# Kernel tuning notes

Hardware: AMD Instinct MI355X
Metric: run time of the kernel (lower is better)

The kernel has to match this reference:

```python
import jax, jax.numpy as jnp
import numpy as np

BS, N_LINKS, MAX_LEN = 8192, 512, 32
D_LINK, D_PATH, D_READ, N_OUT = 32, 128, 256, 3
BN_EPS = 1e-5


def setup_inputs() -> dict:
    key = jax.random.key(0)
    ks = jax.random.split(key, 16)
    capa = jax.random.uniform(ks[0], (BS, N_LINKS), jnp.float32, 0.5, 1.0) * 100.0
    avail = jax.random.uniform(ks[1], (BS, N_LINKS), jnp.float32) * capa
    loss = jax.random.uniform(ks[2], (BS, N_LINKS), jnp.float32) * 0.05
    demand = jax.random.uniform(ks[3], (BS,), jnp.float32) * 10.0
    path = jax.random.randint(ks[4], (BS, MAX_LEN), 0, N_LINKS)
    hop_num = jax.random.randint(ks[5], (BS,), 1, MAX_LEN + 1)
    s = 0.1
    inp = {
        "demand": demand,
        "link_avail_capacity": avail,
        "link_capacity": capa,
        "link_loss": loss,
        "path": path,
        "hop_num": hop_num,
        # GRU params (PyTorch layout: [3H, D] gates ordered r,z,n)
        "gru_w_ih": jax.random.normal(ks[6], (3 * D_PATH, D_LINK), jnp.float32) * s,
        "gru_w_hh": jax.random.normal(ks[7], (3 * D_PATH, D_PATH), jnp.float32) * s,
        "gru_b_ih": jax.random.normal(ks[8], (3 * D_PATH,), jnp.float32) * s,
        "gru_b_hh": jax.random.normal(ks[9], (3 * D_PATH,), jnp.float32) * s,
        "bn_gamma": jnp.ones((D_PATH,), jnp.float32),
        "bn_beta": jnp.zeros((D_PATH,), jnp.float32),
        # stacked readout heads [N_OUT, ...]
        "rW1": jax.random.normal(ks[10], (N_OUT, D_PATH, D_READ), jnp.float32) * s,
        "rb1": jnp.zeros((N_OUT, D_READ), jnp.float32),
        "rW2": jax.random.normal(ks[11], (N_OUT, D_READ, D_READ), jnp.float32) * s,
        "rb2": jnp.zeros((N_OUT, D_READ), jnp.float32),
        "rW3": jax.random.normal(ks[12], (N_OUT, D_READ, 1), jnp.float32) * s,
        "rb3": jnp.zeros((N_OUT, 1), jnp.float32),
    }
    return inp


def _gru_scan(x_bt, h0, w_ih, w_hh, b_ih, b_hh):
    # x_bt: [B, T, D]; h0: [B, H] -> outputs [B, T, H]
    H = h0.shape[-1]
    def step(h, x_t):
        gi = x_t @ w_ih.T + b_ih          # [B, 3H]
        gh = h @ w_hh.T + b_hh            # [B, 3H]
        i_r, i_z, i_n = gi[:, :H], gi[:, H:2*H], gi[:, 2*H:]
        h_r, h_z, h_n = gh[:, :H], gh[:, H:2*H], gh[:, 2*H:]
        r = jax.nn.sigmoid(i_r + h_r)
        z = jax.nn.sigmoid(i_z + h_z)
        n = jnp.tanh(i_n + r * h_n)
        h_new = (1.0 - z) * n + z * h
        return h_new, h_new
    _, outs = jax.lax.scan(step, h0, jnp.swapaxes(x_bt, 0, 1))
    return jnp.swapaxes(outs, 0, 1)


def reference(demand, link_avail_capacity, link_capacity, link_loss, path, hop_num,
              gru_w_ih, gru_w_hh, gru_b_ih, gru_b_hh, bn_gamma, bn_beta,
              rW1, rb1, rW2, rb2, rW3, rb3):
    bs, n_links = link_capacity.shape
    max_len = path.shape[1]
    max_capa = jax.lax.stop_gradient(jnp.max(link_capacity))
    # link_state: [B, n_links, D_LINK]; first D_LINK-4 channels are zeros
    feats = jnp.stack([
        link_avail_capacity / max_capa,
        link_capacity / max_capa,
        link_avail_capacity / link_capacity,
        link_loss,
    ], axis=-1)
    link_state = jnp.concatenate(
        [jnp.zeros((bs, n_links, D_LINK - 4), feats.dtype), feats], axis=-1)
    link_state = jax.lax.stop_gradient(link_state)  # original detaches
    # initial hidden: zeros except last channel = demand/max_capa
    h0 = jnp.concatenate(
        [jnp.zeros((bs, D_PATH - 1), feats.dtype), (demand / max_capa)[:, None]], axis=-1)
    # fused gather of link states along each path, masked past hop_num
    gathered = jnp.take_along_axis(link_state, path[:, :, None], axis=1)  # [B, T, D]
    mask = (jnp.arange(max_len)[None, :] < hop_num[:, None])[:, :, None]
    link_inputs = gathered * mask.astype(gathered.dtype)
    outputs = _gru_scan(link_inputs, h0, gru_w_ih, gru_w_hh, gru_b_ih, gru_b_hh)
    # extract hidden state at last hop of each path
    idx = (hop_num - 1)[:, None, None]
    flow = jnp.take_along_axis(outputs, idx, axis=1)[:, 0, :]  # [B, H]
    # BatchNorm1d (training mode: batch statistics, biased variance)
    mean = jnp.mean(flow, axis=0)
    var = jnp.mean((flow - mean) ** 2, axis=0)
    flow = (flow - mean) * jax.lax.rsqrt(var + BN_EPS) * bn_gamma + bn_beta
    # readout heads: Linear -> SELU -> Linear -> SELU -> Linear
    h1 = jax.nn.selu(jnp.einsum('bh,uhr->ubr', flow, rW1) + rb1[:, None, :])
    h2 = jax.nn.selu(jnp.einsum('ubr,urs->ubs', h1, rW2) + rb2[:, None, :])
    y = jnp.einsum('ubs,uso->ubo', h2, rW3) + rb3[:, None, :]  # [U, B, 1]
    return jnp.transpose(y[:, :, 0], (1, 0))  # [B, U]
```

## Files before the change

### kernel.cpp

```cpp
#include <hip/hip_runtime.h>


#define BS 8192
#define NL 512
#define ML 32
#define DP 128
#define DR 256
#define NJOB 512
#define ST 172

#define OFF_SUM    64
#define OFF_SSQ    192
#define OFF_CUR    576
#define OFF_PERM   640
#define OFF_WHH16  (OFF_PERM + BS)
#define OFF_W1     (OFF_WHH16 + 24576)
#define OFF_W2     (OFF_W1 + 49152)
#define OFF_FEATS  (OFF_W2 + 98304)
#define OFF_FLOW   (OFF_FEATS + BS*ML*4)

#define FEATS_BLOCKS 1024
#define MAX_BLOCKS   256
#define WPREP_BLOCKS 336
#define SORT_BID     (FEATS_BLOCKS + MAX_BLOCKS + WPREP_BLOCKS)
#define SORT_BLOCKS  32
#define PREP_GRID    (SORT_BID + SORT_BLOCKS)

#define KS (-1.44269504088896340736f)
#define KT ( 2.88539008177792681472f)

typedef _Float16 f16x8 __attribute__((ext_vector_type(8)));
typedef _Float16 f16x4 __attribute__((ext_vector_type(4)));
typedef float    f32x4 __attribute__((ext_vector_type(4)));

__device__ __forceinline__ float exp2_raw_(float x){
#if __has_builtin(__builtin_amdgcn_exp2f)
  return __builtin_amdgcn_exp2f(x);
#else
  return exp2f(x);
#endif
}

__device__ __forceinline__ float sig2_(float x){
  return __builtin_amdgcn_rcpf(1.0f + exp2_raw_(x));
}
__device__ __forceinline__ float tanh2_(float v){
  return fmaf(-2.0f, __builtin_amdgcn_rcpf(1.0f + exp2_raw_(v)), 1.0f);
}
__device__ __forceinline__ float seluf_(float x){
  const float sc = 1.0507009873554805f, al = 1.6732632423543772f;
  return x > 0.0f ? sc*x : sc*al*(__expf(x)-1.0f);
}

__global__ void prep_all(const int* __restrict__ path, const int* __restrict__ hop,
                         const float* __restrict__ avail, const float* __restrict__ capa,
                         const float* __restrict__ loss, const float* __restrict__ whh,
                         const float* __restrict__ rW1, const float* __restrict__ rW2,
                         float* ws){
  const int bid = blockIdx.x;
  const int tid = threadIdx.x;

  if (bid < FEATS_BLOCKS){
    int idx = bid*256 + tid;
    int b = idx >> 5, t = idx & 31;
    f16x4 o = (f16x4)0;
    if (t < hop[b]){
      int l = path[idx];
      float a = avail[b*NL + l];
      float c = capa [b*NL + l];
      o[0] = (_Float16)a;
      o[1] = (_Float16)c;
      o[2] = (_Float16)(a / c);
      o[3] = (_Float16)loss[b*NL + l];
    }
    ((f16x4*)((_Float16*)(ws + OFF_FEATS)))[idx] = o;
  } else if (bid < FEATS_BLOCKS + MAX_BLOCKS){
    const float4* c4 = (const float4*)capa;
    const int n4 = BS*NL/4;
    float m = 0.0f;
    for (int i = (bid - FEATS_BLOCKS)*256 + tid; i < n4; i += MAX_BLOCKS*256){
      float4 v = c4[i];
      m = fmaxf(m, fmaxf(fmaxf(v.x, v.y), fmaxf(v.z, v.w)));
    }
    #pragma unroll
    for (int o = 32; o > 0; o >>= 1) m = fmaxf(m, __shfl_down(m, o, 64));
    if ((tid & 63) == 0) atomicMax((int*)ws, __float_as_int(m));
  } else if (bid < SORT_BID){
    _Float16* whh16 = (_Float16*)(ws + OFF_WHH16);
    _Float16* w1    = (_Float16*)(ws + OFF_W1);
    _Float16* w2    = (_Float16*)(ws + OFF_W2);
    int base = (bid - FEATS_BLOCKS - MAX_BLOCKS)*1024 + tid*4;
    if (base < 49152){
      const float s = (base < 32768) ? KS : KT;
      const float4 v = *(const float4*)(whh + base);
      f16x4 o = { (_Float16)(v.x*s), (_Float16)(v.y*s),
                  (_Float16)(v.z*s), (_Float16)(v.w*s) };
      *(f16x4*)(whh16 + base) = o;
    } else if (base < 147456){
      int j = base - 49152;
      int u = j >> 15;        int rem  = j & 32767;
      int ngrp = rem >> 11;   int rem2 = rem & 2047;
      int kc   = rem2 >> 9;   int rem3 = rem2 & 511;
      int l    = rem3 >> 3;   int e0   = rem3 & 7;
      int n = ngrp*16 + (l & 15);
      int k = kc*32 + (l >> 4)*8 + e0;
      const float* src = rW1 + u*32768 + k*256 + n;
      f16x4 o = { (_Float16)src[0], (_Float16)src[256], (_Float16)src[512], (_Float16)src[768] };
      *(f16x4*)(w1 + j) = o;
    } else {
      int j = base - 147456;
      int u = j >> 16;        int rem  = j & 65535;
      int ngrp = rem >> 12;   int rem2 = rem & 4095;
      int kc   = rem2 >> 9;   int rem3 = rem2 & 511;
      int l    = rem3 >> 3;   int e0   = rem3 & 7;
      int n = ngrp*16 + (l & 15);
      int k = kc*32 + (l >> 4)*8 + e0;
      const float* src = rW2 + u*65536 + k*256 + n;
      f16x4 o = { (_Float16)src[0], (_Float16)src[256], (_Float16)src[512], (_Float16)src[768] };
      *(f16x4*)(w2 + j) = o;
    }
  } else {
    const int v  = bid - SORT_BID;
    const int hv = 32 - v;
    __shared__ int wsum[4];
    __shared__ int cur;
    if (v == 0)
      for (int i = 64 + tid; i < 640; i += 256) ws[i] = 0.0f;
    int cnt = 0;
    for (int b = tid; b < BS; b += 256) cnt += (hop[b] > hv) ? 1 : 0;
    #pragma unroll
    for (int o = 32; o > 0; o >>= 1) cnt += __shfl_down(cnt, o, 64);
    if ((tid & 63) == 0) wsum[tid >> 6] = cnt;
    if (tid == 0) cur = 0;
    __syncthreads();
    const int start_v = wsum[0] + wsum[1] + wsum[2] + wsum[3];
    int* perm = (int*)ws + OFF_PERM;
    for (int b = tid; b < BS; b += 256){
      if (hop[b] == hv){
        int p = atomicAdd(&cur, 1);
        perm[start_v + p] = b;
      }
    }
  }
}

__launch_bounds__(256, 2)
__global__ void kgru(const float* __restrict__ demand, const int* __restrict__ hop,
                     const float* __restrict__ wih, const float* __restrict__ bih,
                     const float* __restrict__ bhh, float* __restrict__ ws,
                     float* __restrict__ flow){
  __shared__ _Float16 hA[2][16*ST];
  const int tid  = threadIdx.x;
  const int w    = tid >> 6;
  const int lane = tid & 63;
  const int lm   = lane & 15;
  const int qd   = lane >> 4;
  const int ch0  = w*32 + lm;
  const int ch1  = w*32 + 16 + lm;
  const float inv_maxc = 1.0f / ws[0];
  const int* perm = (const int*)ws + OFF_PERM;
  const f16x4* feats16 = (const f16x4*)((const _Float16*)(ws + OFF_FEATS));
  const _Float16* whh16 = (const _Float16*)(ws + OFF_WHH16);

  const int bid = blockIdx.x;
  const int q = (bid < 256) ? bid : 767 - bid;

  for (int idx = tid; idx < 1024; idx += 256){
    const int buf = idx >> 9;
    const int rem = idx & 511;
    const int m   = rem >> 5;
    const int c   = 128 + (rem & 31);
    hA[buf][m*ST + c] = (_Float16)0.f;
  }

  f16x8 bfr[2][5], bfz[2][5], bfnh[2][4], bfni[2];
  #pragma unroll
  for (int s = 0; s < 2; ++s){
    const int chs = w*32 + s*16 + lm;
    #pragma unroll
    for (int kc = 0; kc < 4; ++kc){
      bfr[s][kc]  = *(const f16x8*)(whh16 + (      chs)*128 + kc*32 + qd*8);
      bfz[s][kc]  = *(const f16x8*)(whh16 + (128 + chs)*128 + kc*32 + qd*8);
      bfnh[s][kc] = *(const f16x8*)(whh16 + (256 + chs)*128 + kc*32 + qd*8);
    }
    bfr[s][4] = (f16x8)0; bfz[s][4] = (f16x8)0; bfni[s] = (f16x8)0;
    if (qd == 0){
      #pragma unroll
      for (int j = 0; j < 4; ++j){
        float sc = (j < 2) ? inv_maxc : 1.0f;
        bfr[s][4][j] = (_Float16)(wih[(      chs)*32 + 28 + j] * sc * KS);
        bfz[s][4][j] = (_Float16)(wih[(128 + chs)*32 + 28 + j] * sc * KS);
        bfni[s][j]   = (_Float16)(wih[(256 + chs)*32 + 28 + j] * sc * KT);
      }
    }
  }
  const float bR0  = (bih[ch0]     + bhh[ch0]    ) * KS;
  const float bR1  = (bih[ch1]     + bhh[ch1]    ) * KS;
  const float bZ0  = (bih[128+ch0] + bhh[128+ch0]) * KS;
  const float bZ1  = (bih[128+ch1] + bhh[128+ch1]) * KS;
  const float bNI0 = bih[256+ch0] * KT;
  const float bNI1 = bih[256+ch1] * KT;
  const float bNH0 = bhh[256+ch0] * KT;
  const float bNH1 = bhh[256+ch1] * KT;

  int it[4], hp[4];
  #pragma unroll
  for (int r = 0; r < 4; ++r){
    it[r] = perm[q*16 + qd*4 + r];
    hp[r] = hop[it[r]];
  }
  int tmax = max(max(hp[0],hp[1]), max(hp[2],hp[3]));
  tmax = max(tmax, __shfl_xor(tmax, 16, 64));
  tmax = max(tmax, __shfl_xor(tmax, 32, 64));

  const int  fw_i = w*4 + lane;
  const bool fw   = (lane < 4);
  const int  fw_b = fw ? perm[q*16 + fw_i] : 0;

  __syncthreads();

  float hprev0[4], hprev1[4];
  #pragma unroll
  for (int r = 0; r < 4; ++r){
    hprev0[r] = 0.0f;
    hprev1[r] = (ch1 == 127) ? demand[it[r]] * inv_maxc : 0.0f;
    hA[0][(qd*4 + r)*ST + ch0] = (_Float16)hprev0[r];
    hA[0][(qd*4 + r)*ST + ch1] = (_Float16)hprev1[r];
  }
  f16x4 fvreg = (f16x4)0;
  if (fw){
    *(f16x4*)(&hA[0][fw_i*ST + 128]) = feats16[fw_b*ML + 0];
    fvreg = feats16[fw_b*ML + 1];
  }
  __syncthreads();

  for (int t = 0; t < tmax; ++t){
    const int cur = t & 1, nxt = cur ^ 1;
    if (fw){
      *(f16x4*)(&hA[nxt][fw_i*ST + 128]) = fvreg;
      int tn = t + 2; tn = (tn < ML) ? tn : (ML - 1);
      fvreg = feats16[fw_b*ML + tn];
    }

    f16x8 a[5];
    #pragma unroll
    for (int kc = 0; kc < 5; ++kc)
      a[kc] = *(const f16x8*)(&hA[cur][lm*ST + kc*32 + qd*8]);

    {
      f32x4 accr  = {bR0, bR0, bR0, bR0};
      f32x4 accz  = {bZ0, bZ0, bZ0, bZ0};
      f32x4 accnh = {bNH0, bNH0, bNH0, bNH0};
      f32x4 accni = {bNI0, bNI0, bNI0, bNI0};
      #pragma unroll
      for (int kc = 0; kc < 5; ++kc){
        accr = __builtin_amdgcn_mfma_f32_16x16x32_f16(a[kc], bfr[0][kc], accr, 0, 0, 0);
        accz = __builtin_amdgcn_mfma_f32_16x16x32_f16(a[kc], bfz[0][kc], accz, 0, 0, 0);
        if (kc < 4)
          accnh = __builtin_amdgcn_mfma_f32_16x16x32_f16(a[kc], bfnh[0][kc], accnh, 0, 0, 0);
        else
          accni = __builtin_amdgcn_mfma_f32_16x16x32_f16(a[kc], bfni[0], accni, 0, 0, 0);
      }
      #pragma unroll
      for (int r = 0; r < 4; ++r){
        float rr = sig2_(accr[r]);
        float zz = sig2_(accz[r]);
        float nn = tanh2_(fmaf(rr, accnh[r], accni[r]));
        float hn = fmaf(zz, hprev0[r] - nn, nn);
        if (t < hp[r]) hprev0[r] = hn;
        hA[nxt][(qd*4 + r)*ST + ch0] = (_Float16)hprev0[r];
      }
    }
    {
      f32x4 accr  = {bR1, bR1, bR1, bR1};
      f32x4 accz  = {bZ1, bZ1, bZ1, bZ1};
      f32x4 accnh = {bNH1, bNH1, bNH1, bNH1};
      f32x4 accni = {bNI1, bNI1, bNI1, bNI1};
      #pragma unroll
      for (int kc = 0; kc < 5; ++kc){
        accr = __builtin_amdgcn_mfma_f32_16x16x32_f16(a[kc], bfr[1][kc], accr, 0, 0, 0);
        accz = __builtin_amdgcn_mfma_f32_16x16x32_f16(a[kc], bfz[1][kc], accz, 0, 0, 0);
        if (kc < 4)
          accnh = __builtin_amdgcn_mfma_f32_16x16x32_f16(a[kc], bfnh[1][kc], accnh, 0, 0, 0);
        else
          accni = __builtin_amdgcn_mfma_f32_16x16x32_f16(a[kc], bfni[1], accni, 0, 0, 0);
      }
      #pragma unroll
      for (int r = 0; r < 4; ++r){
        float rr = sig2_(accr[r]);
        float zz = sig2_(accz[r]);
        float nn = tanh2_(fmaf(rr, accnh[r], accni[r]));
        float hn = fmaf(zz, hprev1[r] - nn, nn);
        if (t < hp[r]) hprev1[r] = hn;
        hA[nxt][(qd*4 + r)*ST + ch1] = (_Float16)hprev1[r];
      }
    }
    __syncthreads();
  }

  float s0 = 0.f, q0 = 0.f, s1 = 0.f, q1 = 0.f;
  #pragma unroll
  for (int r = 0; r < 4; ++r){
    float v0 = hprev0[r], v1 = hprev1[r];
    flow[it[r]*DP + ch0] = v0;
    flow[it[r]*DP + ch1] = v1;
    s0 += v0;  q0 = fmaf(v0, v0, q0);
    s1 += v1;  q1 = fmaf(v1, v1, q1);
  }
  s0 += __shfl_xor(s0, 16, 64);  s0 += __shfl_xor(s0, 32, 64);
  q0 += __shfl_xor(q0, 16, 64);  q0 += __shfl_xor(q0, 32, 64);
  s1 += __shfl_xor(s1, 16, 64);  s1 += __shfl_xor(s1, 32, 64);
  q1 += __shfl_xor(q1, 16, 64);  q1 += __shfl_xor(q1, 32, 64);
  if (qd == 0){
    atomicAdd(&ws[OFF_SUM + ch0], s0);
    atomicAdd(&ws[OFF_SSQ + ch0], q0);
    atomicAdd(&ws[OFF_SUM + ch1], s1);
    atomicAdd(&ws[OFF_SSQ + ch1], q1);
  }
}

__launch_bounds__(256, 4)
__global__ void kmlp(const float* __restrict__ flow, const float* __restrict__ ws,
                     const float* __restrict__ gamma, const float* __restrict__ beta,
                     const float* __restrict__ rb1, const float* __restrict__ rb2,
                     const float* __restrict__ rW3, const float* __restrict__ rb3,
                     float* __restrict__ out){
  __shared__ _Float16 x_lds[32*136];
  __shared__ _Float16 h1_lds[32*264];
  __shared__ float aa[DP], bb[DP];
  __shared__ float y_part[4][32];
  const int tid  = threadIdx.x;
  const int w    = tid >> 6;
  const int lane = tid & 63;
  const int lm   = lane & 15;
  const int qd   = lane >> 4;
  const int b0   = blockIdx.x * 32;
  const int u    = blockIdx.y;
  const _Float16* w1 = (const _Float16*)(ws + OFF_W1) + u*(DR*DP);
  const _Float16* w2 = (const _Float16*)(ws + OFF_W2) + u*(DR*DR);

  if (tid < DP){
    float m = ws[OFF_SUM + tid] * (1.0f/BS);
    float q = ws[OFF_SSQ + tid] * (1.0f/BS);
    float rstd = rsqrtf(q - m*m + 1e-5f);
    float a = rstd * gamma[tid];
    aa[tid] = a;
    bb[tid] = fmaf(-m, a, beta[tid]);
  }
  __syncthreads();

  for (int idx = tid; idx < 32*DP; idx += 256){
    int i = idx >> 7, h = idx & 127;
    x_lds[i*136 + h] = (_Float16)fmaf(flow[(b0 + i)*DP + h], aa[h], bb[h]);
  }
  __syncthreads();

  for (int nt = 0; nt < 4; ++nt){
    const int ng = 4*w + nt;
    const int n  = ng*16 + lm;
    const float bias1 = rb1[u*DR + n];
    f16x8 b1[4];
    #pragma unroll
    for (int kc = 0; kc < 4; ++kc)
      b1[kc] = *(const f16x8*)(w1 + ((ng*4 + kc)*64 + lane)*8);
    #pragma unroll
    for (int mt = 0; mt < 2; ++mt){
      f32x4 acc = {bias1, bias1, bias1, bias1};
      #pragma unroll
      for (int kc = 0; kc < 4; ++kc){
        f16x8 a1 = *(const f16x8*)(&x_lds[(mt*16 + lm)*136 + kc*32 + qd*8]);
        acc = __builtin_amdgcn_mfma_f32_16x16x32_f16(a1, b1[kc], acc, 0, 0, 0);
      }
      #pragma unroll
      for (int r = 0; r < 4; ++r)
        h1_lds[(mt*16 + qd*4 + r)*264 + n] = (_Float16)seluf_(acc[r]);
    }
  }
  __syncthreads();

  {
    float p[2][4] = {{0.f,0.f,0.f,0.f},{0.f,0.f,0.f,0.f}};
    for (int nt = 0; nt < 4; ++nt){
      const int ng = 4*w + nt;
      const int n  = ng*16 + lm;
      const float bias2 = rb2[u*DR + n];
      const float w3l   = rW3[u*DR + n];
      f16x8 b2[8];
      #pragma unroll
      for (int kc = 0; kc < 8; ++kc)
        b2[kc] = *(const f16x8*)(w2 + ((ng*8 + kc)*64 + lane)*8);
      #pragma unroll
      for (int mt = 0; mt < 2; ++mt){
        f32x4 acc = {bias2, bias2, bias2, bias2};
        #pragma unroll
        for (int kc = 0; kc < 8; ++kc){
          f16x8 a2 = *(const f16x8*)(&h1_lds[(mt*16 + lm)*264 + kc*32 + qd*8]);
          acc = __builtin_amdgcn_mfma_f32_16x16x32_f16(a2, b2[kc], acc, 0, 0, 0);
        }
        #pragma unroll
        for (int r = 0; r < 4; ++r)
          p[mt][r] += seluf_(acc[r]) * w3l;
      }
    }
    #pragma unroll
    for (int mt = 0; mt < 2; ++mt){
      #pragma unroll
      for (int r = 0; r < 4; ++r){
        float v = p[mt][r];
        v += __shfl_xor(v, 1, 64);
        v += __shfl_xor(v, 2, 64);
        v += __shfl_xor(v, 4, 64);
        v += __shfl_xor(v, 8, 64);
        if (lm == 0) y_part[w][mt*16 + qd*4 + r] = v;
      }
    }
  }
  __syncthreads();
  if (tid < 32){
    float y = y_part[0][tid] + y_part[1][tid] + y_part[2][tid] + y_part[3][tid] + rb3[u];
    out[(b0 + tid)*3 + u] = y;
  }
}

extern "C" void kernel_launch(void* const* d_in, const int* in_sizes, int n_in,
                              void* d_out, int out_size, void* d_ws, size_t ws_size,
                              hipStream_t stream){
  const float* demand = (const float*)d_in[0];
  const float* avail  = (const float*)d_in[1];
  const float* capa   = (const float*)d_in[2];
  const float* loss   = (const float*)d_in[3];
  const int*   path   = (const int*)d_in[4];
  const int*   hop    = (const int*)d_in[5];
  const float* wih    = (const float*)d_in[6];
  const float* whh    = (const float*)d_in[7];
  const float* bih    = (const float*)d_in[8];
  const float* bhh    = (const float*)d_in[9];
  const float* gamma  = (const float*)d_in[10];
  const float* beta   = (const float*)d_in[11];
  const float* rW1    = (const float*)d_in[12];
  const float* rb1    = (const float*)d_in[13];
  const float* rW2    = (const float*)d_in[14];
  const float* rb2    = (const float*)d_in[15];
  const float* rW3    = (const float*)d_in[16];
  const float* rb3    = (const float*)d_in[17];
  float* ws  = (float*)d_ws;
  float* out = (float*)d_out;

  prep_all <<<PREP_GRID, 256, 0, stream>>>(path, hop, avail, capa, loss,
                                           whh, rW1, rW2, ws);
  kgru     <<<NJOB, 256, 0, stream>>>(demand, hop, wih, bih, bhh, ws, ws + OFF_FLOW);
  kmlp     <<<dim3(BS/32, 3), 256, 0, stream>>>(ws + OFF_FLOW, ws, gamma, beta,
                                                rb1, rb2, rW3, rb3, out);
}
```

Before: 188.6 us.

## Fuse per-path link feature gather and readout weight repack into GRU kernel

The link-state gather along each path moves out of the prep kernel and into the GRU kernel. Each block gathers the features for its 16 sorted items straight into shared memory, which removes the global fp16 feature buffer write and read-back. The readout W1/W2 fp16 repacking also moves into the GRU blocks, so the prep grid shrinks to the max reduction, Whh conversion and the sort. In exchange, every GRU block pays an uncached random gather before its recurrence starts. Masking of timesteps past hop_num is dropped, which relies on only the hop-1 output being extracted.

```diff
diff --git a/kernel.cpp b/kernel.cpp
--- a/kernel.cpp
+++ b/kernel.cpp
@@ -19,10 +19,9 @@
 #define OFF_FEATS  (OFF_W2 + 98304)
 #define OFF_FLOW   (OFF_FEATS + BS*ML*4)
 
-#define FEATS_BLOCKS 1024
 #define MAX_BLOCKS   256
-#define WPREP_BLOCKS 336
-#define SORT_BID     (FEATS_BLOCKS + MAX_BLOCKS + WPREP_BLOCKS)
+#define WHH_BLOCKS   48
+#define SORT_BID     (MAX_BLOCKS + WHH_BLOCKS)
 #define SORT_BLOCKS  32
 #define PREP_GRID    (SORT_BID + SORT_BLOCKS)
 
@@ -60,25 +59,11 @@
   const int bid = blockIdx.x;
   const int tid = threadIdx.x;
 
-  if (bid < FEATS_BLOCKS){
-    int idx = bid*256 + tid;
-    int b = idx >> 5, t = idx & 31;
-    f16x4 o = (f16x4)0;
-    if (t < hop[b]){
-      int l = path[idx];
-      float a = avail[b*NL + l];
-      float c = capa [b*NL + l];
-      o[0] = (_Float16)a;
-      o[1] = (_Float16)c;
-      o[2] = (_Float16)(a / c);
-      o[3] = (_Float16)loss[b*NL + l];
-    }
-    ((f16x4*)((_Float16*)(ws + OFF_FEATS)))[idx] = o;
-  } else if (bid < FEATS_BLOCKS + MAX_BLOCKS){
+  if (bid < MAX_BLOCKS){
     const float4* c4 = (const float4*)capa;
     const int n4 = BS*NL/4;
     float m = 0.0f;
-    for (int i = (bid - FEATS_BLOCKS)*256 + tid; i < n4; i += MAX_BLOCKS*256){
+    for (int i = bid*256 + tid; i < n4; i += MAX_BLOCKS*256){
       float4 v = c4[i];
       m = fmaxf(m, fmaxf(fmaxf(v.x, v.y), fmaxf(v.z, v.w)));
     }
@@ -87,17 +72,91 @@
     if ((tid & 63) == 0) atomicMax((int*)ws, __float_as_int(m));
   } else if (bid < SORT_BID){
     _Float16* whh16 = (_Float16*)(ws + OFF_WHH16);
-    _Float16* w1    = (_Float16*)(ws + OFF_W1);
-    _Float16* w2    = (_Float16*)(ws + OFF_W2);
-    int base = (bid - FEATS_BLOCKS - MAX_BLOCKS)*1024 + tid*4;
-    if (base < 49152){
-      const float s = (base < 32768) ? KS : KT;
-      const float4 v = *(const float4*)(whh + base);
-      f16x4 o = { (_Float16)(v.x*s), (_Float16)(v.y*s),
-                  (_Float16)(v.z*s), (_Float16)(v.w*s) };
-      *(f16x4*)(whh16 + base) = o;
-    } else if (base < 147456){
-      int j = base - 49152;
+    int base = (bid - MAX_BLOCKS)*1024 + tid*4;
+    const float s = (base < 32768) ? KS : KT;
+    const float4 v = *(const float4*)(whh + base);
+    f16x4 o = { (_Float16)(v.x*s), (_Float16)(v.y*s),
+                (_Float16)(v.z*s), (_Float16)(v.w*s) };
+    *(f16x4*)(whh16 + base) = o;
+  } else {
+    const int v  = bid - SORT_BID;
+    const int hv = 32 - v;
+    __shared__ int wsum[4];
+    __shared__ int cur;
+    if (v == 0)
+      for (int i = 64 + tid; i < 640; i += 256) ws[i] = 0.0f;
+    int cnt = 0;
+    for (int b = tid; b < BS; b += 256) cnt += (hop[b] > hv) ? 1 : 0;
+    #pragma unroll
+    for (int o = 32; o > 0; o >>= 1) cnt += __shfl_down(cnt, o, 64);
+    if ((tid & 63) == 0) wsum[tid >> 6] = cnt;
+    if (tid == 0) cur = 0;
+    __syncthreads();
+    const int start_v = wsum[0] + wsum[1] + wsum[2] + wsum[3];
+    int* perm = (int*)ws + OFF_PERM;
+    for (int b = tid; b < BS; b += 256){
+      if (hop[b] == hv){
+        int p = atomicAdd(&cur, 1);
+        perm[start_v + p] = b;
+      }
+    }
+  }
+}
+
+__launch_bounds__(256, 2)
+__global__ void kgru(const float* __restrict__ demand, const int* __restrict__ hop,
+                     const float* __restrict__ wih, const float* __restrict__ bih,
+                     const float* __restrict__ bhh,
+                     const float* __restrict__ avail, const float* __restrict__ capa,
+                     const float* __restrict__ loss, const int* __restrict__ path,
+                     const float* __restrict__ rW1, const float* __restrict__ rW2,
+                     float* __restrict__ ws, float* __restrict__ flow){
+  __shared__ _Float16 hA[2][16*ST];
+  __shared__ __align__(8) _Float16 feats_l[16*33*4];
+  __shared__ int bl_it[16], bl_hp[16];
+  const int tid  = threadIdx.x;
+  const int w    = tid >> 6;
+  const int lane = tid & 63;
+  const int lm   = lane & 15;
+  const int qd   = lane >> 4;
+  const int ch0  = w*32 + lm;
+  const int ch1  = w*32 + 16 + lm;
+  const float inv_maxc = 1.0f / ws[0];
+  const int* perm = (const int*)ws + OFF_PERM;
+  const _Float16* whh16 = (const _Float16*)(ws + OFF_WHH16);
+
+  const int bid = blockIdx.x;
+  const int q = (bid < 256) ? bid : 767 - bid;
+
+  for (int idx = tid; idx < 1024; idx += 256){
+    const int buf = idx >> 9;
+    const int rem = idx & 511;
+    const int m   = rem >> 5;
+    const int c   = 128 + (rem & 31);
+    hA[buf][m*ST + c] = (_Float16)0.f;
+  }
+  if (tid < 16){ int b = perm[q*16 + tid]; bl_it[tid] = b; bl_hp[tid] = hop[b]; }
+  __syncthreads();
+
+  #pragma unroll
+  for (int j = 0; j < 2; ++j){
+    int u = tid + j*256;
+    int item = u >> 5, t = u & 31;
+    int b = bl_it[item];
+    int l = path[b*ML + t];
+    float a  = avail[b*NL + l];
+    float c  = capa [b*NL + l];
+    float lo = loss [b*NL + l];
+    f16x4 o = { (_Float16)a, (_Float16)c, (_Float16)(a / c), (_Float16)lo };
+    *(f16x4*)(&feats_l[(item*33 + t)*4]) = o;
+  }
+
+  if (tid < 144){
+    _Float16* w1 = (_Float16*)(ws + OFF_W1);
+    _Float16* w2 = (_Float16*)(ws + OFF_W2);
+    int base = (bid*144 + tid)*4;
+    if (base < 98304){
+      int j = base;
       int u = j >> 15;        int rem  = j & 32767;
       int ngrp = rem >> 11;   int rem2 = rem & 2047;
       int kc   = rem2 >> 9;   int rem3 = rem2 & 511;
@@ -108,7 +167,7 @@
       f16x4 o = { (_Float16)src[0], (_Float16)src[256], (_Float16)src[512], (_Float16)src[768] };
       *(f16x4*)(w1 + j) = o;
     } else {
-      int j = base - 147456;
+      int j = base - 98304;
       int u = j >> 16;        int rem  = j & 65535;
       int ngrp = rem >> 12;   int rem2 = rem & 4095;
       int kc   = rem2 >> 9;   int rem3 = rem2 & 511;
@@ -119,58 +178,6 @@
       f16x4 o = { (_Float16)src[0], (_Float16)src[256], (_Float16)src[512], (_Float16)src[768] };
       *(f16x4*)(w2 + j) = o;
     }
-  } else {
-    const int v  = bid - SORT_BID;
-    const int hv = 32 - v;
-    __shared__ int wsum[4];
-    __shared__ int cur;
-    if (v == 0)
-      for (int i = 64 + tid; i < 640; i += 256) ws[i] = 0.0f;
-    int cnt = 0;
-    for (int b = tid; b < BS; b += 256) cnt += (hop[b] > hv) ? 1 : 0;
-    #pragma unroll
-    for (int o = 32; o > 0; o >>= 1) cnt += __shfl_down(cnt, o, 64);
-    if ((tid & 63) == 0) wsum[tid >> 6] = cnt;
-    if (tid == 0) cur = 0;
-    __syncthreads();
-    const int start_v = wsum[0] + wsum[1] + wsum[2] + wsum[3];
-    int* perm = (int*)ws + OFF_PERM;
-    for (int b = tid; b < BS; b += 256){
-      if (hop[b] == hv){
-        int p = atomicAdd(&cur, 1);
-        perm[start_v + p] = b;
-      }
-    }
-  }
-}
-
-__launch_bounds__(256, 2)
-__global__ void kgru(const float* __restrict__ demand, const int* __restrict__ hop,
-                     const float* __restrict__ wih, const float* __restrict__ bih,
-                     const float* __restrict__ bhh, float* __restrict__ ws,
-                     float* __restrict__ flow){
-  __shared__ _Float16 hA[2][16*ST];
-  const int tid  = threadIdx.x;
-  const int w    = tid >> 6;
-  const int lane = tid & 63;
-  const int lm   = lane & 15;
-  const int qd   = lane >> 4;
-  const int ch0  = w*32 + lm;
-  const int ch1  = w*32 + 16 + lm;
-  const float inv_maxc = 1.0f / ws[0];
-  const int* perm = (const int*)ws + OFF_PERM;
-  const f16x4* feats16 = (const f16x4*)((const _Float16*)(ws + OFF_FEATS));
-  const _Float16* whh16 = (const _Float16*)(ws + OFF_WHH16);
-
-  const int bid = blockIdx.x;
-  const int q = (bid < 256) ? bid : 767 - bid;
-
-  for (int idx = tid; idx < 1024; idx += 256){
-    const int buf = idx >> 9;
-    const int rem = idx & 511;
-    const int m   = rem >> 5;
-    const int c   = 128 + (rem & 31);
-    hA[buf][m*ST + c] = (_Float16)0.f;
   }
 
   f16x8 bfr[2][5], bfz[2][5], bfnh[2][4], bfni[2];
@@ -206,8 +213,8 @@
   int it[4], hp[4];
   #pragma unroll
   for (int r = 0; r < 4; ++r){
-    it[r] = perm[q*16 + qd*4 + r];
-    hp[r] = hop[it[r]];
+    it[r] = bl_it[qd*4 + r];
+    hp[r] = bl_hp[qd*4 + r];
   }
   int tmax = max(max(hp[0],hp[1]), max(hp[2],hp[3]));
   tmax = max(tmax, __shfl_xor(tmax, 16, 64));
@@ -215,7 +222,6 @@
 
   const int  fw_i = w*4 + lane;
   const bool fw   = (lane < 4);
-  const int  fw_b = fw ? perm[q*16 + fw_i] : 0;
 
   __syncthreads();
 
@@ -227,20 +233,15 @@
     hA[0][(qd*4 + r)*ST + ch0] = (_Float16)hprev0[r];
     hA[0][(qd*4 + r)*ST + ch1] = (_Float16)hprev1[r];
   }
-  f16x4 fvreg = (f16x4)0;
-  if (fw){
-    *(f16x4*)(&hA[0][fw_i*ST + 128]) = feats16[fw_b*ML + 0];
-    fvreg = feats16[fw_b*ML + 1];
-  }
+  if (fw)
+    *(f16x4*)(&hA[0][fw_i*ST + 128]) = *(const f16x4*)(&feats_l[(fw_i*33)*4]);
   __syncthreads();
 
   for (int t = 0; t < tmax; ++t){
     const int cur = t & 1, nxt = cur ^ 1;
-    if (fw){
-      *(f16x4*)(&hA[nxt][fw_i*ST + 128]) = fvreg;
-      int tn = t + 2; tn = (tn < ML) ? tn : (ML - 1);
-      fvreg = feats16[fw_b*ML + tn];
-    }
+    if (fw && (t+1) < ML)
+      *(f16x4*)(&hA[nxt][fw_i*ST + 128]) =
+          *(const f16x4*)(&feats_l[(fw_i*33 + t + 1)*4]);
 
     f16x8 a[5];
     #pragma unroll
@@ -448,7 +449,9 @@
 
   prep_all <<<PREP_GRID, 256, 0, stream>>>(path, hop, avail, capa, loss,
                                            whh, rW1, rW2, ws);
-  kgru     <<<NJOB, 256, 0, stream>>>(demand, hop, wih, bih, bhh, ws, ws + OFF_FLOW);
+  kgru     <<<NJOB, 256, 0, stream>>>(demand, hop, wih, bih, bhh,
+                                      avail, capa, loss, path, rW1, rW2,
+                                      ws, ws + OFF_FLOW);
   kmlp     <<<dim3(BS/32, 3), 256, 0, stream>>>(ws + OFF_FLOW, ws, gamma, beta,
                                                 rb1, rb2, rW3, rb3, out);
 }
```

New measurement: 191.7 us. About the same (+1.7%).
